# Optimization experiments

Hardware: AMD Instinct MI355X
Metric: run time of the kernel (lower is better)

Reference implementation:

```python
import jax, jax.numpy as jnp
import numpy as np
from jax import lax

NMS_THRESH = 0.5
BN_EPS = 1e-5
TO_REMOVE = 1.0  # neural-motifs box convention (+1 in width/height)


def nms_overlaps(boxes):
    # boxes: [N, C, 4] xyxy -> per-class pairwise IoU [N, N, C]
    x1 = jnp.maximum(boxes[:, None, :, 0], boxes[None, :, :, 0])
    y1 = jnp.maximum(boxes[:, None, :, 1], boxes[None, :, :, 1])
    x2 = jnp.minimum(boxes[:, None, :, 2], boxes[None, :, :, 2])
    y2 = jnp.minimum(boxes[:, None, :, 3], boxes[None, :, :, 3])
    inter = jnp.clip(x2 - x1 + TO_REMOVE, 0.0) * jnp.clip(y2 - y1 + TO_REMOVE, 0.0)
    area = (boxes[:, :, 2] - boxes[:, :, 0] + TO_REMOVE) * (boxes[:, :, 3] - boxes[:, :, 1] + TO_REMOVE)  # [N,C]
    union = area[:, None, :] + area[None, :, :] - inter
    return inter / union


def greedy_nms_labels(obj_dists, is_overlap):
    # faithful port of nms_per_cls: iterative argmax + per-class suppression
    N, C = obj_dists.shape
    scores = jax.nn.softmax(obj_dists, axis=-1)
    scores = scores.at[:, 0].set(-1.0)  # kill background column

    def step(carry, _):
        scores, labels = carry
        flat = jnp.argmax(scores)          # row-major, same as np.unravel_index
        box_ind = flat // C
        cls_ind = flat % C
        labels = labels.at[box_ind].set(cls_ind.astype(jnp.int32))
        ov = is_overlap[box_ind, :, cls_ind]  # [N] bool
        col = jnp.where(ov, 0.0, scores[:, cls_ind])
        scores = scores.at[:, cls_ind].set(col)
        scores = scores.at[box_ind, :].set(-1.0)
        return (scores, labels), None

    (_, labels), _ = lax.scan(step, (scores, jnp.zeros(N, jnp.int32)), None, length=N)
    return labels


def setup_inputs() -> dict:
    key = jax.random.key(0)
    ks = jax.random.split(key, 16)
    N, C, D, E, H, P = 400, 151, 4096, 200, 512, 128
    x = jax.random.normal(ks[0], (N, D), jnp.float32)
    predict_logits = jax.random.normal(ks[1], (N, C), jnp.float32) * 2.0
    pos_input = jax.random.uniform(ks[2], (N, 9), jnp.float32)
    xy = jax.random.uniform(ks[3], (N, C, 2), jnp.float32) * 800.0
    wh = jax.random.uniform(ks[4], (N, C, 2), jnp.float32) * 200.0 + 1.0
    boxes_per_cls = jnp.concatenate([xy, xy + wh], axis=-1)
    sc = lambda k, sh: jax.random.normal(k, sh, jnp.float32) * np.float32(1.0 / np.sqrt(sh[0]))
    return {
        'x': x,
        'predict_logits': predict_logits,
        'pos_input': pos_input,
        'boxes_per_cls': boxes_per_cls,
        'obj_embed_w': jax.random.normal(ks[5], (C, E), jnp.float32) * 0.1,
        'obj_embed2_w': jax.random.normal(ks[6], (C, E), jnp.float32) * 0.1,
        'w_pos1': sc(ks[7], (9, 32)), 'b_pos1': jnp.zeros(32, jnp.float32),
        'bn_gamma': jnp.ones(32, jnp.float32), 'bn_beta': jnp.zeros(32, jnp.float32),
        'bn_mean': jnp.zeros(32, jnp.float32), 'bn_var': jnp.ones(32, jnp.float32),
        'w_pos2': sc(ks[8], (32, P)), 'b_pos2': jnp.zeros(P, jnp.float32),
        'w_lin': sc(ks[9], (D + E + P, H)), 'b_lin': jnp.zeros(H, jnp.float32),
        'w_out': sc(ks[10], (H, C)), 'b_out': jnp.zeros(C, jnp.float32),
        'w_fc': sc(ks[11], (D + E + P, H)), 'b_fc': jnp.zeros(H, jnp.float32),
    }


def reference(x, predict_logits, pos_input, boxes_per_cls, obj_embed_w, obj_embed2_w,
              w_pos1, b_pos1, bn_gamma, bn_beta, bn_mean, bn_var, w_pos2, b_pos2,
              w_lin, b_lin, w_out, b_out, w_fc, b_fc):
    # sgdet inference path of VTransEFeaturePE.forward
    obj_embed = jax.nn.softmax(predict_logits, axis=-1) @ obj_embed_w           # [N,E]
    h = pos_input @ w_pos1 + b_pos1                                             # Linear(9,32)
    h = (h - bn_mean) / jnp.sqrt(bn_var + BN_EPS) * bn_gamma + bn_beta          # BN eval
    pos_embed = jax.nn.relu(h @ w_pos2 + b_pos2)                                # [N,128]
    rep = jnp.concatenate([x, obj_embed, pos_embed], axis=-1)                   # [N,4424]
    obj_dists = (rep @ w_lin + b_lin) @ w_out + b_out                           # [N,C]
    is_overlap = nms_overlaps(boxes_per_cls) >= NMS_THRESH                      # [N,N,C]
    obj_preds = greedy_nms_labels(obj_dists, is_overlap)                        # [N] int32
    obj_embed2 = obj_embed2_w[obj_preds]                                        # [N,E]
    obj_rel_rep = jnp.concatenate([x, pos_embed, obj_embed2], axis=-1)
    edge_ctx = jax.nn.relu(obj_rel_rep @ w_fc + b_fc)                           # [N,H]
    return (obj_dists, obj_preds, edge_ctx)
```

## Files before the change

### kernel.cpp

```cpp
#include <hip/hip_runtime.h>
#include <hip/hip_bf16.h>
#include <stdint.h>

#define NB 400
#define NC 151
#define DX 4096
#define DE 200
#define DP 128
#define DH 512
#define KREP 4424
#define TAILW 328
#define MPAD 416
#define SPLITK 8
#define TILES1 139
#define TILES2 132
#define SKSTRIDE 152

__device__ __forceinline__ uint32_t f2ord(float f) {
  uint32_t u = __float_as_uint(f);
  return (u & 0x80000000u) ? ~u : (u | 0x80000000u);
}

__global__ __launch_bounds__(256) void k_embed(
    const float* __restrict__ logits, const float* __restrict__ obj_embed_w,
    const float* __restrict__ pos_input, const float* __restrict__ w_pos1,
    const float* __restrict__ b_pos1, const float* __restrict__ bn_gamma,
    const float* __restrict__ bn_beta, const float* __restrict__ bn_mean,
    const float* __restrict__ bn_var, const float* __restrict__ w_pos2,
    const float* __restrict__ b_pos2, float* __restrict__ tail1) {
  int r = blockIdx.x, t = threadIdx.x;
  if (r >= NB) {
    if (t < TAILW) tail1[r * TAILW + t] = 0.f;
    return;
  }
  __shared__ float p[NC];
  __shared__ float red[256];
  __shared__ float hb[32];

  float v = (t < NC) ? logits[r * NC + t] : -INFINITY;
  red[t] = v; __syncthreads();
  for (int s = 128; s > 0; s >>= 1) { if (t < s) red[t] = fmaxf(red[t], red[t + s]); __syncthreads(); }
  float m = red[0]; __syncthreads();
  float e = (t < NC) ? expf(v - m) : 0.f;
  red[t] = e; __syncthreads();
  for (int s = 128; s > 0; s >>= 1) { if (t < s) red[t] += red[t + s]; __syncthreads(); }
  float sum = red[0];
  if (t < NC) p[t] = e / sum;

  if (t < 32) {
    float acc = b_pos1[t];
    for (int k = 0; k < 9; k++) acc += pos_input[r * 9 + k] * w_pos1[k * 32 + t];
    acc = (acc - bn_mean[t]) / sqrtf(bn_var[t] + 1e-5f) * bn_gamma[t] + bn_beta[t];
    hb[t] = acc;
  }
  __syncthreads();

  if (t < DE) {
    float acc = 0.f;
    for (int k = 0; k < NC; k++) acc += p[k] * obj_embed_w[k * DE + t];
    tail1[r * TAILW + t] = acc;
  }
  if (t < DP) {
    float acc = b_pos2[t];
    for (int k = 0; k < 32; k++) acc += hb[k] * w_pos2[k * DP + t];
    tail1[r * TAILW + DE + t] = fmaxf(acc, 0.f);
  }
}

__device__ __forceinline__ void gemm_body(
    float (*As)[36], float (*Bs)[68],
    const float* __restrict__ x, const float* __restrict__ tail,
    const float* __restrict__ w, float* __restrict__ part,
    int bid, int tiles, int toff) {
  int tid = threadIdx.x;
  int n0 = (bid & 7) * 64, m0 = ((bid >> 3) % 13) * 32;
  int z = bid / 104;
  int tbeg = (z * tiles) / SPLITK, tend = ((z + 1) * tiles) / SPLITK;
  int ty = tid >> 4, tx = tid & 15;
  int a_r = tid >> 3, a_c = (tid & 7) << 2;
  int b_r = tid >> 4, b_c = (tid & 15) << 2;
  float4 acc0 = {0, 0, 0, 0}, acc1 = {0, 0, 0, 0};

  auto loadA = [&](int t) -> float4 {
    int k = t * 32 + a_c;
    int row = m0 + a_r;
    float4 v = {0, 0, 0, 0};
    if (k < KREP) {
      if (k < DX) { if (row < NB) v = *(const float4*)&x[(size_t)row * DX + k]; }
      else v = *(const float4*)&tail[row * TAILW + toff + (k - DX)];
    }
    return v;
  };
  auto loadB = [&](int t, int roff) -> float4 {
    int k = t * 32 + b_r + roff;
    float4 v = {0, 0, 0, 0};
    if (k < KREP) v = *(const float4*)&w[(size_t)k * DH + n0 + b_c];
    return v;
  };

  float4 pa = loadA(tbeg), pb0 = loadB(tbeg, 0), pb1 = loadB(tbeg, 16);
  for (int t = tbeg; t < tend; t++) {
    __syncthreads();
    *(float4*)&As[a_r][a_c] = pa;
    *(float4*)&Bs[b_r][b_c] = pb0;
    *(float4*)&Bs[b_r + 16][b_c] = pb1;
    __syncthreads();
    if (t + 1 < tend) { pa = loadA(t + 1); pb0 = loadB(t + 1, 0); pb1 = loadB(t + 1, 16); }
#pragma unroll
    for (int k4 = 0; k4 < 8; k4++) {
      float4 a0 = *(float4*)&As[ty * 2][k4 * 4];
      float4 a1 = *(float4*)&As[ty * 2 + 1][k4 * 4];
#pragma unroll
      for (int j = 0; j < 4; j++) {
        float4 bv = *(float4*)&Bs[k4 * 4 + j][tx * 4];
        float av0 = (&a0.x)[j], av1 = (&a1.x)[j];
        acc0.x += av0 * bv.x; acc0.y += av0 * bv.y; acc0.z += av0 * bv.z; acc0.w += av0 * bv.w;
        acc1.x += av1 * bv.x; acc1.y += av1 * bv.y; acc1.z += av1 * bv.z; acc1.w += av1 * bv.w;
      }
    }
  }
  int row0 = m0 + ty * 2, col = n0 + tx * 4;
  float* base = part + (size_t)z * NB * DH;
  if (row0 < NB)     *(float4*)&base[row0 * DH + col] = acc0;
  if (row0 + 1 < NB) *(float4*)&base[(row0 + 1) * DH + col] = acc1;
}

__global__ __launch_bounds__(256) void k_g1ov(
    const float* __restrict__ x, const float* __restrict__ tail1,
    const float* __restrict__ w_lin, float* __restrict__ part,
    const float* __restrict__ boxes, uint64_t* __restrict__ ov_bits) {
  __shared__ __align__(16) float As[32][36];
  __shared__ __align__(16) float Bs[32][68];
  int bid = blockIdx.x;
  if (bid >= 832) {
    int c = bid - 832;
    int t = threadIdx.x;
    __shared__ float4 bx[NB];
    const float4* bp4 = (const float4*)boxes;
    for (int j = t; j < NB; j += 256) bx[j] = bp4[j * NC + c];
    __syncthreads();
    int wave = t >> 6, lane = t & 63;
    for (int b = wave; b < NB; b += 4) {
      float4 A = bx[b];
      float areaA = (A.z - A.x + 1.f) * (A.w - A.y + 1.f);
      for (int chunk = 0; chunk < 7; chunk++) {
        int j = chunk * 64 + lane;
        bool ov = false;
        if (j < NB) {
          float4 B = bx[j];
          float x1 = fmaxf(A.x, B.x), y1 = fmaxf(A.y, B.y);
          float x2 = fminf(A.z, B.z), y2 = fminf(A.w, B.w);
          float iw = fmaxf(x2 - x1 + 1.f, 0.f), ih = fmaxf(y2 - y1 + 1.f, 0.f);
          float inter = iw * ih;
          float areaB = (B.z - B.x + 1.f) * (B.w - B.y + 1.f);
          ov = (inter / (areaA + areaB - inter)) >= 0.5f;
        }
        uint64_t mask = __ballot(ov);
        if (lane == 0) ov_bits[((size_t)(b * NC + c) << 3) + chunk] = mask;
      }
    }
    return;
  }
  gemm_body(As, Bs, x, tail1, w_lin, part, bid, TILES1, 0);
}

__global__ __launch_bounds__(256) void k_dists(
    const float* __restrict__ part, const float* __restrict__ b_lin,
    const float* __restrict__ w_out, const float* __restrict__ b_out,
    float* __restrict__ out_dists, uint64_t* __restrict__ skeys) {
  int r = blockIdx.x, t = threadIdx.x;
  __shared__ float h[DH];
  __shared__ float red[256];
  __shared__ float sval[NC];
  float s0 = b_lin[t], s1 = b_lin[t + 256];
#pragma unroll
  for (int z = 0; z < SPLITK; z++) {
    const float* pr = part + ((size_t)z * NB + r) * DH;
    s0 += pr[t]; s1 += pr[t + 256];
  }
  h[t] = s0; h[t + 256] = s1;
  __syncthreads();

  float acc = -INFINITY;
  if (t < NC) {
    acc = b_out[t];
    for (int k = 0; k < DH; k++) acc += h[k] * w_out[k * NC + t];
    out_dists[r * NC + t] = acc;
  }
  red[t] = (t < NC) ? acc : -INFINITY; __syncthreads();
  for (int s = 128; s > 0; s >>= 1) { if (t < s) red[t] = fmaxf(red[t], red[t + s]); __syncthreads(); }
  float mx = red[0]; __syncthreads();
  float e = (t < NC) ? expf(acc - mx) : 0.f;
  red[t] = e; __syncthreads();
  for (int s = 128; s > 0; s >>= 1) { if (t < s) red[t] += red[t + s]; __syncthreads(); }
  float sum = red[0];
  if (t < NC) sval[t] = e / sum;
  __syncthreads();

  if (t >= 1 && t < NC) {
    float v = sval[t];
    int rank = 0;
    for (int c2 = 1; c2 < NC; c2++) {
      float v2 = sval[c2];
      rank += (v2 > v) || (v2 == v && c2 < t);
    }
    skeys[(size_t)r * SKSTRIDE + rank] =
        ((uint64_t)f2ord(v) << 17) | ((uint64_t)(511 - r) << 8) | (uint64_t)t;
  }
}

struct GemmSm { float As[32][36]; float Bs[32][68]; };
struct NmsSm  { uint64_t top4[2][4][4]; };

__global__ __launch_bounds__(256) void k_nms_g2a(
    const uint64_t* __restrict__ ov_bits, const uint64_t* __restrict__ skeys,
    int* __restrict__ labels_g, float* __restrict__ out_preds,
    const float* __restrict__ x, const float* __restrict__ tail1,
    const float* __restrict__ w_fc, float* __restrict__ part) {
  __shared__ __align__(16) union { GemmSm g; NmsSm n; } sm;
  if (blockIdx.x > 0) {
    gemm_body(sm.g.As, sm.g.Bs, x, tail1, w_fc, part, blockIdx.x - 1, TILES2, DE);
    return;
  }
  int tid = threadIdx.x, wave = tid >> 6, lane = tid & 63;
  int S0w = wave * 2;
  uint64_t cand[2];
  uint64_t supp0[2], supp1[2], supp2[2];
  int depth[2];
  bool removed[2];
  int reszmin[2];

#pragma unroll
  for (int u = 0; u < 2; u++) {
    int r = (S0w + u) * 64 + lane;
    supp0[u] = supp1[u] = supp2[u] = 0;
    depth[u] = 0; removed[u] = false; reszmin[u] = 255;
    if (r < NB) {
      cand[u] = skeys[(size_t)r * SKSTRIDE];
      labels_g[r] = 0; out_preds[r] = 0.f;
    } else cand[u] = 0;
  }

  auto cswap = [](uint64_t& a, uint64_t& b) {
    uint64_t hi = a > b ? a : b, lo = a > b ? b : a; a = hi; b = lo;
  };

  int picked = 0, rr = 0;
  while (picked < NB) {
    int pp = rr & 1; rr++;
    uint64_t k0 = cand[0] > cand[1] ? cand[0] : cand[1];
    uint64_t k1 = cand[0] > cand[1] ? cand[1] : cand[0];
    uint64_t k2 = 0, k3 = 0;
#pragma unroll
    for (int off = 1; off < 64; off <<= 1) {
      uint64_t p0 = (uint64_t)__shfl_xor((unsigned long long)k0, off, 64);
      uint64_t p1 = (uint64_t)__shfl_xor((unsigned long long)k1, off, 64);
      uint64_t p2 = (uint64_t)__shfl_xor((unsigned long long)k2, off, 64);
      uint64_t p3 = (uint64_t)__shfl_xor((unsigned long long)k3, off, 64);
      uint64_t t0 = k0 > p3 ? k0 : p3;
      uint64_t t1 = k1 > p2 ? k1 : p2;
      uint64_t t2 = k2 > p1 ? k2 : p1;
      uint64_t t3 = k3 > p0 ? k3 : p0;
      cswap(t0, t2); cswap(t1, t3); cswap(t0, t1); cswap(t2, t3);
      k0 = t0; k1 = t1; k2 = t2; k3 = t3;
    }
    if (lane < 4) {
      uint64_t kv = (lane == 0) ? k0 : (lane == 1) ? k1 : (lane == 2) ? k2 : k3;
      sm.n.top4[pp][wave][lane] = kv;
    }
    __syncthreads();

    uint64_t A0 = sm.n.top4[pp][0][0], A1 = sm.n.top4[pp][0][1], A2 = sm.n.top4[pp][0][2], A3 = sm.n.top4[pp][0][3];
    uint64_t B0 = sm.n.top4[pp][1][0], B1 = sm.n.top4[pp][1][1], B2 = sm.n.top4[pp][1][2], B3 = sm.n.top4[pp][1][3];
    uint64_t C0 = sm.n.top4[pp][2][0], C1 = sm.n.top4[pp][2][1], C2 = sm.n.top4[pp][2][2], C3 = sm.n.top4[pp][2][3];
    uint64_t D0 = sm.n.top4[pp][3][0], D1 = sm.n.top4[pp][3][1], D2 = sm.n.top4[pp][3][2], D3 = sm.n.top4[pp][3][3];
    uint64_t x0 = A0, x1 = A1, x2 = A2, x3 = A3, x4 = B3, x5 = B2, x6 = B1, x7 = B0;
    cswap(x0,x4); cswap(x1,x5); cswap(x2,x6); cswap(x3,x7);
    cswap(x0,x2); cswap(x1,x3); cswap(x4,x6); cswap(x5,x7);
    cswap(x0,x1); cswap(x2,x3); cswap(x4,x5); cswap(x6,x7);
    uint64_t y0 = C0, y1 = C1, y2 = C2, y3 = C3, y4 = D3, y5 = D2, y6 = D1, y7 = D0;
    cswap(y0,y4); cswap(y1,y5); cswap(y2,y6); cswap(y3,y7);
    cswap(y0,y2); cswap(y1,y3); cswap(y4,y6); cswap(y5,y7);
    cswap(y0,y1); cswap(y2,y3); cswap(y4,y5); cswap(y6,y7);
    uint64_t tk[8];
    tk[0] = x0 > y7 ? x0 : y7;  tk[1] = x1 > y6 ? x1 : y6;
    tk[2] = x2 > y5 ? x2 : y5;  tk[3] = x3 > y4 ? x3 : y4;
    tk[4] = x4 > y3 ? x4 : y3;  tk[5] = x5 > y2 ? x5 : y2;
    tk[6] = x6 > y1 ? x6 : y1;  tk[7] = x7 > y0 ? x7 : y0;
    cswap(tk[0],tk[4]); cswap(tk[1],tk[5]); cswap(tk[2],tk[6]); cswap(tk[3],tk[7]);
    cswap(tk[0],tk[2]); cswap(tk[1],tk[3]); cswap(tk[4],tk[6]); cswap(tk[5],tk[7]);
    cswap(tk[0],tk[1]); cswap(tk[2],tk[3]); cswap(tk[4],tk[5]); cswap(tk[6],tk[7]);

    int cntA = 0, cntB = 0, cntC = 0, cntD = 0;
#pragma unroll
    for (int i = 0; i < 8; i++) {
      cntA += (tk[i] > A3); cntB += (tk[i] > B3);
      cntC += (tk[i] > C3); cntD += (tk[i] > D3);
    }
    int mincnt = cntA < cntB ? cntA : cntB;
    mincnt = mincnt < cntC ? mincnt : cntC;
    mincnt = mincnt < cntD ? mincnt : cntD;

    int npick = NB - picked; if (npick > 8) npick = 8;

    int pi = lane >> 3, pw = lane & 7;
    int bsel = 0, csel = 0;
#pragma unroll
    for (int i = 0; i < 8; i++)
      if (pi == i) {
        bsel = 511 - (int)((tk[i] >> 8) & 0x1FF);
        csel = (int)(tk[i] & 0xFF);
      }
    uint64_t wv = 0;
    if (pi < npick && pw < 7)
      wv = ov_bits[(((size_t)(bsel * NC + csel)) << 3) + pw];
    uint32_t packed = ((uint32_t)bsel << 8) | (uint32_t)csel;

    uint64_t balnz_raw = __ballot(wv != 0ull);

    uint64_t ovall = 0;
#pragma unroll
    for (int j = 0; j < 8; j++) {
      int bj = 511 - (int)((tk[j] >> 8) & 0x1FF);
      bool hit = (pw == (bj >> 6)) && ((wv >> (bj & 63)) & 1);
      uint64_t bal = __ballot(hit);
      bal |= bal >> 4; bal |= bal >> 2; bal |= bal >> 1;
      uint32_t m8 = (uint32_t)(((bal & 0x0101010101010101ULL) * 0x0102040810204080ULL) >> 56);
      ovall |= (uint64_t)m8 << (8 * j);
    }

    int napply = 1; bool stop = false;
#pragma unroll
    for (int j = 1; j < 8; j++) {
      bool bad = (j >= npick) || (j > mincnt) ||
                 ((uint32_t)(tk[j] >> 17) <= 0x80000000u);
      int cjv = (int)(tk[j] & 0xFF);
#pragma unroll
      for (int i = 0; i < j; i++)
        bad = bad || (((int)(tk[i] & 0xFF) == cjv) && ((ovall >> (8 * j + i)) & 1));
      stop = stop || bad;
      if (!stop) napply = j + 1;
    }

    uint64_t am = (napply >= 8) ? ~0ull : ((1ull << (8 * napply)) - 1);
    uint64_t balnz = balnz_raw & am;

#pragma unroll
    for (int u = 0; u < 2; u++) {
      int S = S0w + u;
      int r = S * 64 + lane;
      for (int i = 0; i < napply; i++) {
        int bc = __shfl((int)packed, i * 8, 64);
        int b = (bc >> 8) & 0x1FF, c = bc & 0xFF;
        bool act = ((balnz >> (i * 8 + S)) & 1) || ((b >> 6) == S);
        if (!act) continue;
        uint64_t owv = (uint64_t)__shfl((unsigned long long)wv, i * 8 + S, 64);
        if (r == b) {
          removed[u] = true; reszmin[u] = 255;
          cand[u] = ((uint64_t)0x407FFFFFu << 17) | ((uint64_t)(511 - r) << 8);
          labels_g[b] = c; out_preds[b] = (float)c;
        } else if ((owv >> lane) & 1) {
          if (removed[u]) {
            if (c < reszmin[u]) reszmin[u] = c;
            cand[u] = ((uint64_t)0x80000000u << 17) | ((uint64_t)(511 - r) << 8)
                      | (uint64_t)reszmin[u];
          } else {
            uint64_t bit = 1ull << (c & 63);
            if (c < 64) supp0[u] |= bit; else if (c < 128) supp1[u] |= bit; else supp2[u] |= bit;
            if ((int)(cand[u] & 0xFF) == c) {
              int d = depth[u] + 1;
              uint64_t k = 0;
              for (; d < 150; d++) {
                k = skeys[(size_t)r * SKSTRIDE + d];
                int col = (int)(k & 0xFF);
                uint64_t mm = (col < 64) ? supp0[u] : ((col < 128) ? supp1[u] : supp2[u]);
                if (!((mm >> (col & 63)) & 1)) break;
              }
              if (d >= 150)
                k = ((uint64_t)0x80000000u << 17) | ((uint64_t)(511 - r) << 8) | 1ull;
              depth[u] = d; cand[u] = k;
            }
          }
        }
      }
    }
    picked += napply;
  }
}

__global__ __launch_bounds__(256) void k_final(
    const float* __restrict__ emb2, const int* __restrict__ labels,
    const float* __restrict__ w_fc, const float* __restrict__ part,
    const float* __restrict__ b_fc, float* __restrict__ out_edge) {
  __shared__ __align__(16) float As[32][36];
  __shared__ __align__(16) float Bs[32][68];
  int tid = threadIdx.x;
  int n0 = blockIdx.x * 64, m0 = blockIdx.y * 32;
  int ty = tid >> 4, tx = tid & 15;
  int a_r = tid >> 3, a_c = (tid & 7) << 2;
  int b_r = tid >> 4, b_c = (tid & 15) << 2;
  float4 acc0 = {0, 0, 0, 0}, acc1 = {0, 0, 0, 0};
  int row_a = m0 + a_r;
  int lab = (row_a < NB) ? labels[row_a] : 0;

  auto loadA = [&](int t) -> float4 {
    int kk = t * 32 + a_c;
    float4 v = {0, 0, 0, 0};
    if (kk < DE && row_a < NB) v = *(const float4*)&emb2[(size_t)lab * DE + kk];
    return v;
  };
  auto loadB = [&](int t, int roff) -> float4 {
    int kk = t * 32 + b_r + roff;
    float4 v = {0, 0, 0, 0};
    if (kk < DE) v = *(const float4*)&w_fc[(size_t)(DX + DP + kk) * DH + n0 + b_c];
    return v;
  };

  float4 pa = loadA(0), pb0 = loadB(0, 0), pb1 = loadB(0, 16);
  for (int t = 0; t < 7; t++) {
    __syncthreads();
    *(float4*)&As[a_r][a_c] = pa;
    *(float4*)&Bs[b_r][b_c] = pb0;
    *(float4*)&Bs[b_r + 16][b_c] = pb1;
    __syncthreads();
    if (t + 1 < 7) { pa = loadA(t + 1); pb0 = loadB(t + 1, 0); pb1 = loadB(t + 1, 16); }
#pragma unroll
    for (int k4 = 0; k4 < 8; k4++) {
      float4 a0 = *(float4*)&As[ty * 2][k4 * 4];
      float4 a1 = *(float4*)&As[ty * 2 + 1][k4 * 4];
#pragma unroll
      for (int j = 0; j < 4; j++) {
        float4 bv = *(float4*)&Bs[k4 * 4 + j][tx * 4];
        float av0 = (&a0.x)[j], av1 = (&a1.x)[j];
        acc0.x += av0 * bv.x; acc0.y += av0 * bv.y; acc0.z += av0 * bv.z; acc0.w += av0 * bv.w;
        acc1.x += av1 * bv.x; acc1.y += av1 * bv.y; acc1.z += av1 * bv.z; acc1.w += av1 * bv.w;
      }
    }
  }
  int row0 = m0 + ty * 2, col = n0 + tx * 4;
#pragma unroll
  for (int z = 0; z < SPLITK; z++) {
    if (row0 < NB) {
      float4 p = *(const float4*)&part[((size_t)z * NB + row0) * DH + col];
      acc0.x += p.x; acc0.y += p.y; acc0.z += p.z; acc0.w += p.w;
    }
    if (row0 + 1 < NB) {
      float4 p = *(const float4*)&part[((size_t)z * NB + row0 + 1) * DH + col];
      acc1.x += p.x; acc1.y += p.y; acc1.z += p.z; acc1.w += p.w;
    }
  }
  float4 bv = *(const float4*)&b_fc[col];
  if (row0 < NB) {
    float4 r;
    r.x = fmaxf(acc0.x + bv.x, 0.f); r.y = fmaxf(acc0.y + bv.y, 0.f);
    r.z = fmaxf(acc0.z + bv.z, 0.f); r.w = fmaxf(acc0.w + bv.w, 0.f);
    *(float4*)&out_edge[row0 * DH + col] = r;
  }
  if (row0 + 1 < NB) {
    float4 r;
    r.x = fmaxf(acc1.x + bv.x, 0.f); r.y = fmaxf(acc1.y + bv.y, 0.f);
    r.z = fmaxf(acc1.z + bv.z, 0.f); r.w = fmaxf(acc1.w + bv.w, 0.f);
    *(float4*)&out_edge[(row0 + 1) * DH + col] = r;
  }
}

extern "C" void kernel_launch(void* const* d_in, const int* in_sizes, int n_in,
                              void* d_out, int out_size, void* d_ws, size_t ws_size,
                              hipStream_t stream) {
  const float* x            = (const float*)d_in[0];
  const float* logits       = (const float*)d_in[1];
  const float* pos_input    = (const float*)d_in[2];
  const float* boxes        = (const float*)d_in[3];
  const float* obj_embed_w  = (const float*)d_in[4];
  const float* obj_embed2_w = (const float*)d_in[5];
  const float* w_pos1       = (const float*)d_in[6];
  const float* b_pos1       = (const float*)d_in[7];
  const float* bn_gamma     = (const float*)d_in[8];
  const float* bn_beta      = (const float*)d_in[9];
  const float* bn_mean      = (const float*)d_in[10];
  const float* bn_var       = (const float*)d_in[11];
  const float* w_pos2       = (const float*)d_in[12];
  const float* b_pos2       = (const float*)d_in[13];
  const float* w_lin        = (const float*)d_in[14];
  const float* b_lin        = (const float*)d_in[15];
  const float* w_out        = (const float*)d_in[16];
  const float* b_out        = (const float*)d_in[17];
  const float* w_fc         = (const float*)d_in[18];
  const float* b_fc         = (const float*)d_in[19];

  float* ws         = (float*)d_ws;
  float* tail1      = ws;
  int* labels       = (int*)(tail1 + MPAD * TAILW);
  uint64_t* skeys   = (uint64_t*)(labels + MPAD);
  uint64_t* ov_bits = skeys + (size_t)NB * SKSTRIDE;
  float* part       = (float*)(ov_bits + (size_t)NB * NC * 8);

  float* out       = (float*)d_out;
  float* out_dists = out;
  float* out_preds = out + NB * NC;
  float* out_edge  = out + NB * NC + NB;

  k_embed<<<MPAD, 256, 0, stream>>>(logits, obj_embed_w, pos_input, w_pos1, b_pos1,
                                    bn_gamma, bn_beta, bn_mean, bn_var, w_pos2, b_pos2,
                                    tail1);
  k_g1ov<<<983, 256, 0, stream>>>(x, tail1, w_lin, part, boxes, ov_bits);
  k_dists<<<NB, 256, 0, stream>>>(part, b_lin, w_out, b_out, out_dists, skeys);
  k_nms_g2a<<<833, 256, 0, stream>>>(ov_bits, skeys, labels, out_preds,
                                     x, tail1, w_fc, part);
  k_final<<<dim3(8, 13), 256, 0, stream>>>(obj_embed2_w, labels, w_fc, part,
                                           b_fc, out_edge);
}
```

Before: 585.2 us.

## Batch multiple greedy NMS picks in the zero-score tie phase

Adds a per-wave ballot of rows already marked removed, stored in shared memory, and a separate batching rule for the phase where the top candidate score is exactly zero. In that phase, several picks per iteration can be committed when ordering and tie-break conditions, derived from overlap bits and the smallest removed overlapping row, prove that the sequential argmax would choose the same boxes. The aim is to cut the number of serial NMS iterations once scores reach zero, at the cost of extra shuffles, a ballot and a shared-memory write on every iteration, and a tricky correctness argument.

```diff
diff --git a/kernel.cpp b/kernel.cpp
--- a/kernel.cpp
+++ b/kernel.cpp
@@ -210,7 +210,7 @@
 }
 
 struct GemmSm { float As[32][36]; float Bs[32][68]; };
-struct NmsSm  { uint64_t top4[2][4][4]; };
+struct NmsSm  { uint64_t top4[2][4][4]; uint64_t dmask[2][8]; };
 
 __global__ __launch_bounds__(256) void k_nms_g2a(
     const uint64_t* __restrict__ ov_bits, const uint64_t* __restrict__ skeys,
@@ -268,6 +268,9 @@
       uint64_t kv = (lane == 0) ? k0 : (lane == 1) ? k1 : (lane == 2) ? k2 : k3;
       sm.n.top4[pp][wave][lane] = kv;
     }
+    uint64_t dm0 = __ballot((uint32_t)(cand[0] >> 17) == 0x407FFFFFu);
+    uint64_t dm1 = __ballot((uint32_t)(cand[1] >> 17) == 0x407FFFFFu);
+    if (lane < 2) sm.n.dmask[pp][S0w + lane] = (lane == 0) ? dm0 : dm1;
     __syncthreads();
 
     uint64_t A0 = sm.n.top4[pp][0][0], A1 = sm.n.top4[pp][0][1], A2 = sm.n.top4[pp][0][2], A3 = sm.n.top4[pp][0][3];
@@ -329,17 +332,49 @@
       ovall |= (uint64_t)m8 << (8 * j);
     }
 
+    uint32_t v0 = (uint32_t)(tk[0] >> 17);
     int napply = 1; bool stop = false;
-#pragma unroll
-    for (int j = 1; j < 8; j++) {
-      bool bad = (j >= npick) || (j > mincnt) ||
-                 ((uint32_t)(tk[j] >> 17) <= 0x80000000u);
-      int cjv = (int)(tk[j] & 0xFF);
-#pragma unroll
-      for (int i = 0; i < j; i++)
-        bad = bad || (((int)(tk[i] & 0xFF) == cjv) && ((ovall >> (8 * j + i)) & 1));
-      stop = stop || bad;
-      if (!stop) napply = j + 1;
+    if (v0 > 0x80000000u) {
+#pragma unroll
+      for (int j = 1; j < 8; j++) {
+        bool bad = (j >= npick) || (j > mincnt) ||
+                   ((uint32_t)(tk[j] >> 17) <= 0x80000000u);
+        int cjv = (int)(tk[j] & 0xFF);
+#pragma unroll
+        for (int i = 0; i < j; i++)
+          bad = bad || (((int)(tk[i] & 0xFF) == cjv) && ((ovall >> (8 * j + i)) & 1));
+        stop = stop || bad;
+        if (!stop) napply = j + 1;
+      }
+    } else if (v0 == 0x80000000u) {
+      uint64_t rm = (pw < 7) ? sm.n.dmask[pp][pw] : 0;
+      uint64_t dbits = wv & rm;
+      int minr = dbits ? (pw * 64 + __builtin_ctzll(dbits)) : 1024;
+      {
+        int o = __shfl_xor(minr, 1, 64); minr = o < minr ? o : minr;
+        o = __shfl_xor(minr, 2, 64);     minr = o < minr ? o : minr;
+        o = __shfl_xor(minr, 4, 64);     minr = o < minr ? o : minr;
+      }
+      int mr[8];
+#pragma unroll
+      for (int i = 0; i < 8; i++) mr[i] = __shfl(minr, i * 8, 64);
+#pragma unroll
+      for (int j = 1; j < 8; j++) {
+        int bj = 511 - (int)((tk[j] >> 8) & 0x1FF);
+        int cjv = (int)(tk[j] & 0xFF);
+        bool bad = (j >= npick) || (j > mincnt) ||
+                   ((uint32_t)(tk[j] >> 17) != 0x80000000u);
+#pragma unroll
+        for (int ip = 0; ip < 7; ip++)
+          bad = bad || (ip < j - 1 && ((ovall >> (8 * ip + (j - 1))) & 1));
+#pragma unroll
+        for (int i = 0; i < j; i++) {
+          bad = bad || (mr[i] <= bj);
+          bad = bad || (((ovall >> (8 * j + i)) & 1) && ((int)(tk[i] & 0xFF) < cjv));
+        }
+        stop = stop || bad;
+        if (!stop) napply = j + 1;
+      }
     }
 
     uint64_t am = (napply >= 8) ? ~0ull : ((1ull << (8 * napply)) - 1);
```

Result: slower. 620.5 us (+6.0%).

## Exit batched NMS loop early and finish zero-score tail in single wave

Applied to the files above, without the earlier changes.

The main batched top-k NMS loop now breaks once the best remaining candidate has a zero or suppressed score. The remaining picks are then resolved by a single-wave bitmask loop that orders boxes by index and applies overlap masks from ov_bits. This avoids running the full multi-wave merge and sort machinery for the degenerate tail of picks. The cost is extra shared-memory state and a serial tail loop whose tie-break semantics must exactly match the reference.

```diff
diff --git a/kernel.cpp b/kernel.cpp
--- a/kernel.cpp
+++ b/kernel.cpp
@@ -210,7 +210,8 @@
 }
 
 struct GemmSm { float As[32][36]; float Bs[32][68]; };
-struct NmsSm  { uint64_t top4[2][4][4]; };
+struct NmsSm  { uint64_t top4[2][4][4]; uint64_t amask[8]; uint64_t rmask[8];
+                uint8_t rcol[512]; };
 
 __global__ __launch_bounds__(256) void k_nms_g2a(
     const uint64_t* __restrict__ ov_bits, const uint64_t* __restrict__ skeys,
@@ -290,6 +291,8 @@
     cswap(tk[0],tk[4]); cswap(tk[1],tk[5]); cswap(tk[2],tk[6]); cswap(tk[3],tk[7]);
     cswap(tk[0],tk[2]); cswap(tk[1],tk[3]); cswap(tk[4],tk[6]); cswap(tk[5],tk[7]);
     cswap(tk[0],tk[1]); cswap(tk[2],tk[3]); cswap(tk[4],tk[5]); cswap(tk[6],tk[7]);
+
+    if ((uint32_t)(tk[0] >> 17) <= 0x80000000u) break;
 
     int cntA = 0, cntB = 0, cntC = 0, cntD = 0;
 #pragma unroll
@@ -386,6 +389,91 @@
     }
     picked += napply;
   }
+
+  if (picked < NB) {
+#pragma unroll
+    for (int u = 0; u < 2; u++) {
+      int r = (S0w + u) * 64 + lane;
+      uint64_t am = __ballot(r < NB && !removed[u]);
+      uint64_t rm = __ballot(removed[u] &&
+                             (uint32_t)(cand[u] >> 17) == 0x80000000u);
+      sm.n.rcol[(S0w + u) * 64 + lane] = (uint8_t)reszmin[u];
+      if (lane == 0) { sm.n.amask[S0w + u] = am; sm.n.rmask[S0w + u] = rm; }
+    }
+    __syncthreads();
+    if (wave != 0) return;
+
+    uint64_t A[8], R[8];
+    uint32_t rc[8];
+#pragma unroll
+    for (int s = 0; s < 8; s++) {
+      A[s] = sm.n.amask[s];
+      R[s] = sm.n.rmask[s];
+      rc[s] = sm.n.rcol[s * 64 + lane];
+    }
+
+    while (picked < NB) {
+      int b = 0, sstar = 0; bool found = false;
+#pragma unroll
+      for (int s = 0; s < 8; s++) {
+        uint64_t cm = A[s] | R[s];
+        if (!found && cm != 0ull) {
+          found = true; sstar = s;
+          b = s * 64 + (int)__builtin_ctzll(cm);
+        }
+      }
+      bool fromA = false;
+      uint32_t colv = 0;
+      if (found) {
+#pragma unroll
+        for (int s = 0; s < 8; s++)
+          if (s == sstar) fromA = (A[s] >> (b & 63)) & 1ull;
+        if (fromA) colv = 1;
+        else {
+          uint32_t cv = 0;
+#pragma unroll
+          for (int s = 0; s < 8; s++) {
+            uint32_t v = (uint32_t)__shfl((int)rc[s], b & 63, 64);
+            if (s == sstar) cv = v;
+          }
+          colv = cv;
+        }
+      }
+      uint64_t w = 0;
+      if (lane < 7) w = ov_bits[(((size_t)(b * NC + (int)colv)) << 3) + lane];
+      uint64_t W[8];
+#pragma unroll
+      for (int s = 0; s < 8; s++)
+        W[s] = (uint64_t)__shfl((unsigned long long)w, s, 64);
+      uint64_t T[8];
+#pragma unroll
+      for (int s = 0; s < 8; s++) {
+        uint64_t valid = (s < 6) ? ~0ull : ((s == 6) ? 0xFFFFull : 0ull);
+        T[s] = W[s] & valid & ~A[s];
+      }
+#pragma unroll
+      for (int s = 0; s < 8; s++)
+        if (s == sstar) T[s] &= ~(1ull << (b & 63));
+#pragma unroll
+      for (int s = 0; s < 8; s++)
+        if (s == sstar) {
+          if (fromA) A[s] &= ~(1ull << (b & 63));
+          else       R[s] &= ~(1ull << (b & 63));
+        }
+#pragma unroll
+      for (int s = 0; s < 8; s++) {
+        R[s] |= T[s];
+        if ((T[s] >> lane) & 1ull) rc[s] = rc[s] < colv ? rc[s] : colv;
+      }
+      if (!fromA) {
+#pragma unroll
+        for (int s = 0; s < 8; s++)
+          if (s == sstar && lane == (b & 63)) rc[s] = 255;
+      }
+      if (lane == 0) { labels_g[b] = (int)colv; out_preds[b] = (float)colv; }
+      picked++;
+    }
+  }
 }
 
 __global__ __launch_bounds__(256) void k_final(
```

After: 566.5 us. -3.2%, faster.
